# Kernel tuning notes

Hardware: AMD Instinct MI355X
Metric: run time of the kernel (lower is better)

## Reference

```python
import jax, jax.numpy as jnp
import numpy as np

B, T, C = 512, 256, 384  # batch, seq (<= block_size 256), n_embed
HEAD = 64


def setup_inputs() -> dict:
    key = jax.random.key(0)
    k1, k2, k3, k4 = jax.random.split(key, 4)
    scale = 1.0 / np.sqrt(C)
    return {
        "x": jax.random.normal(k1, (B, T, C), dtype=jnp.float32),
        "Wq": jax.random.normal(k2, (C, HEAD), dtype=jnp.float32) * scale,
        "Wk": jax.random.normal(k3, (C, HEAD), dtype=jnp.float32) * scale,
        "Wv": jax.random.normal(k4, (C, HEAD), dtype=jnp.float32) * scale,
    }


def reference(x, Wq, Wk, Wv):
    # Single causal self-attention head (dropout in eval mode / identity).
    _, T_, C_ = x.shape
    q = x @ Wq  # [B,T,H]
    k = x @ Wk  # [B,T,H]
    v = x @ Wv  # [B,T,H]
    # NOTE: original scales by n_embed**-0.5 (C), not head_size**-0.5.
    wei = jnp.einsum('bth,bsh->bts', q, k) * (C_ ** -0.5)  # [B,T,T]
    causal = jnp.tril(jnp.ones((T_, T_), dtype=bool))
    wei = jnp.where(causal, wei, -jnp.inf)
    wei = jax.nn.softmax(wei, axis=-1)
    return jnp.einsum('bts,bsh->bth', wei, v)  # [B,T,H]
```

## Files before the change

### kernel.cpp

```cpp
#include <hip/hip_runtime.h>

#define B_ 512
#define T_ 256
#define C_ 384
#define H_ 64

typedef __attribute__((ext_vector_type(8))) short bf16x8;
typedef __attribute__((ext_vector_type(4))) float f32x4;

__device__ __forceinline__ short f2bf(float f) {
    unsigned u = __float_as_uint(f);
    u += 0x7fffu + ((u >> 16) & 1u);
    return (short)(u >> 16);
}

__device__ __forceinline__ bf16x8 cvt8(const float* p) {
    const float4* p4 = (const float4*)p;
    float4 a = p4[0], b = p4[1];
    bf16x8 r;
    r[0] = f2bf(a.x); r[1] = f2bf(a.y); r[2] = f2bf(a.z); r[3] = f2bf(a.w);
    r[4] = f2bf(b.x); r[5] = f2bf(b.y); r[6] = f2bf(b.z); r[7] = f2bf(b.w);
    return r;
}

__global__ void pack_w_kernel(const float* __restrict__ Wq, const float* __restrict__ Wk,
                              const float* __restrict__ Wv, short* __restrict__ wp) {
    int p = blockIdx.x * 256 + threadIdx.x;
    if (p >= 12 * 12 * 512) return;
    int j    = p & 7;
    int lane = (p >> 3) & 63;
    int pc   = p >> 9;
    int ct = pc % 12, ks = pc / 12;
    int n  = ct * 16 + (lane & 15);
    int kk = ks * 32 + (lane >> 4) * 8 + j;
    const float* src = (n < 64) ? Wq : ((n < 128) ? Wk : Wv);
    wp[p] = f2bf(src[kk * 64 + (n & 63)]);
}

__global__ __launch_bounds__(256, 3) void qkv_kernel(
    const float* __restrict__ x, const short* __restrict__ wp,
    short* __restrict__ qo, short* __restrict__ ko, short* __restrict__ vo) {
    __shared__ short wtile[12 * 64 * 8];

    const int tid  = threadIdx.x;
    const int lane = tid & 63, w = tid >> 6;
    const int cl = lane & 15, quad = lane >> 4;
    const int rowbase = blockIdx.x * 128;

    const float* xr0 = x + (long)(rowbase + w * 32 + cl) * C_;
    const float* xr1 = xr0 + 16 * C_;

    f32x4 acc[2][12];
    #pragma unroll
    for (int rt = 0; rt < 2; rt++)
        #pragma unroll
        for (int ct = 0; ct < 12; ct++) {
            f32x4 z = {0.f, 0.f, 0.f, 0.f};
            acc[rt][ct] = z;
        }

    for (int ks = 0; ks < 12; ks++) {
        __syncthreads();
        const uint4* src = (const uint4*)(wp + ks * 6144);
        uint4* dst = (uint4*)wtile;
        #pragma unroll
        for (int i = 0; i < 3; i++)
            dst[tid + i * 256] = src[tid + i * 256];
        __syncthreads();

        const int koff = ks * 32 + quad * 8;
        bf16x8 a0 = cvt8(xr0 + koff);
        bf16x8 a1 = cvt8(xr1 + koff);
        #pragma unroll
        for (int ct = 0; ct < 12; ct++) {
            bf16x8 bf = *(const bf16x8*)(wtile + (ct * 64 + lane) * 8);
            acc[0][ct] = __builtin_amdgcn_mfma_f32_16x16x32_bf16(a0, bf, acc[0][ct], 0, 0, 0);
            acc[1][ct] = __builtin_amdgcn_mfma_f32_16x16x32_bf16(a1, bf, acc[1][ct], 0, 0, 0);
        }
    }

    #pragma unroll
    for (int rt = 0; rt < 2; rt++) {
        const int gb = rowbase + w * 32 + rt * 16 + quad * 4;
        #pragma unroll
        for (int ct = 0; ct < 12; ct++) {
            const int n = ct * 16 + cl;
            short* dstp = (n < 64) ? qo : ((n < 128) ? ko : vo);
            const int nn = n & 63;
            #pragma unroll
            for (int r = 0; r < 4; r++)
                dstp[(long)(gb + r) * 64 + nn] = f2bf(acc[rt][ct][r]);
        }
    }
}

__global__ __launch_bounds__(512, 4) void attn_kernel(
    const short* __restrict__ qi, const short* __restrict__ ki,
    const short* __restrict__ vi, float* __restrict__ out) {
    __shared__ short Vs[64 * 264];
    __shared__ short Pb[8][16 * 40];

    const int b = blockIdx.x;
    const int tid = threadIdx.x;
    const int w = tid >> 6, lane = tid & 63;
    const int cl = lane & 15, quad = lane >> 4;

    const short* vb = vi + b * (T_ * H_);
    for (int i = tid; i < (T_ * H_ / 4); i += 512) {
        const int e = i * 4;
        const int t = e >> 6, h = e & 63;
        short4 val = *(const short4*)(vb + e);
        Vs[(h + 0) * 264 + t] = val.x;
        Vs[(h + 1) * 264 + t] = val.y;
        Vs[(h + 2) * 264 + t] = val.z;
        Vs[(h + 3) * 264 + t] = val.w;
    }
    __syncthreads();

    const float scale = 0.05103103630798287f;

    for (int it = 0; it < 2; it++) {
        const int rg = it ? (15 - w) : w;
        const int base = rg << 4;

        const short* qb = qi + (long)(b * T_ + base + cl) * H_;
        const bf16x8 qf0 = *(const bf16x8*)(qb + quad * 8);
        const bf16x8 qf1 = *(const bf16x8*)(qb + 32 + quad * 8);

        f32x4 sacc[16];
        #pragma unroll
        for (int st = 0; st < 16; st++) {
            if (st > rg) continue;
            const short* kb = ki + (long)(b * T_ + st * 16 + cl) * H_;
            bf16x8 k0 = *(const bf16x8*)(kb + quad * 8);
            bf16x8 k1 = *(const bf16x8*)(kb + 32 + quad * 8);
            f32x4 z = {0.f, 0.f, 0.f, 0.f};
            f32x4 t = __builtin_amdgcn_mfma_f32_16x16x32_bf16(qf0, k0, z, 0, 0, 0);
            t = __builtin_amdgcn_mfma_f32_16x16x32_bf16(qf1, k1, t, 0, 0, 0);
            sacc[st] = t;
        }

        float m4[4] = {-3e38f, -3e38f, -3e38f, -3e38f};
        #pragma unroll
        for (int st = 0; st < 16; st++) {
            if (st > rg) continue;
            #pragma unroll
            for (int r = 0; r < 4; r++) {
                float sv = sacc[st][r] * scale;
                if (st * 16 + cl > base + quad * 4 + r) sv = -1e30f;
                sacc[st][r] = sv;
                m4[r] = fmaxf(m4[r], sv);
            }
        }
        #pragma unroll
        for (int d = 1; d < 16; d <<= 1)
            #pragma unroll
            for (int r = 0; r < 4; r++)
                m4[r] = fmaxf(m4[r], __shfl_xor(m4[r], d));

        float l4[4] = {0.f, 0.f, 0.f, 0.f};
        #pragma unroll
        for (int st = 0; st < 16; st++) {
            if (st > rg) continue;
            #pragma unroll
            for (int r = 0; r < 4; r++) {
                float pv = exp2f((sacc[st][r] - m4[r]) * 1.4426950408889634f);
                sacc[st][r] = pv;
                l4[r] += pv;
            }
        }
        #pragma unroll
        for (int d = 1; d < 16; d <<= 1)
            #pragma unroll
            for (int r = 0; r < 4; r++)
                l4[r] += __shfl_xor(l4[r], d);

        f32x4 oacc[4];
        #pragma unroll
        for (int ht = 0; ht < 4; ht++) {
            f32x4 z = {0.f, 0.f, 0.f, 0.f};
            oacc[ht] = z;
        }
        short* pb = Pb[w];
        #pragma unroll
        for (int c = 0; c < 8; c++) {
            if (c > (rg >> 1)) continue;
            #pragma unroll
            for (int half = 0; half < 2; half++) {
                const int st = c * 2 + half;
                #pragma unroll
                for (int r = 0; r < 4; r++) {
                    short pv = (st <= rg) ? f2bf(sacc[st][r]) : (short)0;
                    pb[(quad * 4 + r) * 40 + half * 16 + cl] = pv;
                }
            }
            __builtin_amdgcn_wave_barrier();
            const bf16x8 pa = *(const bf16x8*)(pb + cl * 40 + quad * 8);
            #pragma unroll
            for (int ht = 0; ht < 4; ht++) {
                const bf16x8 vf = *(const bf16x8*)(Vs + (ht * 16 + cl) * 264 + c * 32 + quad * 8);
                oacc[ht] = __builtin_amdgcn_mfma_f32_16x16x32_bf16(pa, vf, oacc[ht], 0, 0, 0);
            }
            __builtin_amdgcn_wave_barrier();
        }

        #pragma unroll
        for (int r = 0; r < 4; r++) {
            const float inv = 1.0f / l4[r];
            float* op = out + (long)(b * T_ + base + quad * 4 + r) * H_ + cl;
            #pragma unroll
            for (int ht = 0; ht < 4; ht++)
                op[ht * 16] = oacc[ht][r] * inv;
        }
    }
}

extern "C" void kernel_launch(void* const* d_in, const int* in_sizes, int n_in,
                              void* d_out, int out_size, void* d_ws, size_t ws_size,
                              hipStream_t stream) {
    const float* x  = (const float*)d_in[0];
    const float* Wq = (const float*)d_in[1];
    const float* Wk = (const float*)d_in[2];
    const float* Wv = (const float*)d_in[3];
    float* out = (float*)d_out;

    short* ws = (short*)d_ws;
    const long QKV = (long)B_ * T_ * H_;
    short* q  = ws;
    short* k  = ws + QKV;
    short* v  = ws + 2 * QKV;
    short* wp = ws + 3 * QKV;

    pack_w_kernel<<<288, 256, 0, stream>>>(Wq, Wk, Wv, wp);
    qkv_kernel<<<(B_ * T_) / 128, 256, 0, stream>>>(x, wp, q, k, v);
    attn_kernel<<<B_, 512, 0, stream>>>(q, k, v, out);
}
```

Before: 350.7 us.

## Split attention blocks per batch and read QKV weights directly from global

The QKV projection kernel drops its shared-memory weight staging and the two barriers per k-step, loading packed bf16 weight fragments straight from global/L2 instead. Its occupancy hint is lowered from 3 to 2 blocks. The attention kernel now runs two 256-thread blocks per batch, each handling half of the row groups, and the V transpose into LDS is rewritten to use vectorized shared-memory stores. This raises the block count and removes sync overhead, but it duplicates the V load and transpose across both blocks of a batch and may raise global load traffic in the projection.

```diff
diff --git a/kernel.cpp b/kernel.cpp
--- a/kernel.cpp
+++ b/kernel.cpp
@@ -37,11 +37,9 @@
     wp[p] = f2bf(src[kk * 64 + (n & 63)]);
 }
 
-__global__ __launch_bounds__(256, 3) void qkv_kernel(
+__global__ __launch_bounds__(256, 2) void qkv_kernel(
     const float* __restrict__ x, const short* __restrict__ wp,
     short* __restrict__ qo, short* __restrict__ ko, short* __restrict__ vo) {
-    __shared__ short wtile[12 * 64 * 8];
-
     const int tid  = threadIdx.x;
     const int lane = tid & 63, w = tid >> 6;
     const int cl = lane & 15, quad = lane >> 4;
@@ -59,21 +57,15 @@
             acc[rt][ct] = z;
         }
 
+    const short* wl = wp + lane * 8;
     for (int ks = 0; ks < 12; ks++) {
-        __syncthreads();
-        const uint4* src = (const uint4*)(wp + ks * 6144);
-        uint4* dst = (uint4*)wtile;
-        #pragma unroll
-        for (int i = 0; i < 3; i++)
-            dst[tid + i * 256] = src[tid + i * 256];
-        __syncthreads();
-
         const int koff = ks * 32 + quad * 8;
         bf16x8 a0 = cvt8(xr0 + koff);
         bf16x8 a1 = cvt8(xr1 + koff);
+        const short* wk = wl + ks * 6144;
         #pragma unroll
         for (int ct = 0; ct < 12; ct++) {
-            bf16x8 bf = *(const bf16x8*)(wtile + (ct * 64 + lane) * 8);
+            bf16x8 bf = *(const bf16x8*)(wk + ct * 512);
             acc[0][ct] = __builtin_amdgcn_mfma_f32_16x16x32_bf16(a0, bf, acc[0][ct], 0, 0, 0);
             acc[1][ct] = __builtin_amdgcn_mfma_f32_16x16x32_bf16(a1, bf, acc[1][ct], 0, 0, 0);
         }
@@ -94,33 +86,35 @@
     }
 }
 
-__global__ __launch_bounds__(512, 4) void attn_kernel(
+__global__ __launch_bounds__(256, 3) void attn_kernel(
     const short* __restrict__ qi, const short* __restrict__ ki,
     const short* __restrict__ vi, float* __restrict__ out) {
     __shared__ short Vs[64 * 264];
-    __shared__ short Pb[8][16 * 40];
-
-    const int b = blockIdx.x;
+    __shared__ short Pb[4][16 * 40];
+
+    const int b = blockIdx.x >> 1;
+    const int ph = blockIdx.x & 1;
     const int tid = threadIdx.x;
     const int w = tid >> 6, lane = tid & 63;
     const int cl = lane & 15, quad = lane >> 4;
 
     const short* vb = vi + b * (T_ * H_);
-    for (int i = tid; i < (T_ * H_ / 4); i += 512) {
-        const int e = i * 4;
-        const int t = e >> 6, h = e & 63;
-        short4 val = *(const short4*)(vb + e);
-        Vs[(h + 0) * 264 + t] = val.x;
-        Vs[(h + 1) * 264 + t] = val.y;
-        Vs[(h + 2) * 264 + t] = val.z;
-        Vs[(h + 3) * 264 + t] = val.w;
+    for (int i = tid; i < (T_ * H_ / 4); i += 256) {
+        const int h = i & 63, tg = i >> 6;
+        short4 val;
+        val.x = vb[(tg * 4 + 0) * 64 + h];
+        val.y = vb[(tg * 4 + 1) * 64 + h];
+        val.z = vb[(tg * 4 + 2) * 64 + h];
+        val.w = vb[(tg * 4 + 3) * 64 + h];
+        *(short4*)(Vs + h * 264 + tg * 4) = val;
     }
     __syncthreads();
 
     const float scale = 0.05103103630798287f;
 
     for (int it = 0; it < 2; it++) {
-        const int rg = it ? (15 - w) : w;
+        const int rg0 = ph * 4 + w;
+        const int rg = it ? (15 - rg0) : rg0;
         const int base = rg << 4;
 
         const short* qb = qi + (long)(b * T_ + base + cl) * H_;
@@ -233,5 +227,5 @@
 
     pack_w_kernel<<<288, 256, 0, stream>>>(Wq, Wk, Wv, wp);
     qkv_kernel<<<(B_ * T_) / 128, 256, 0, stream>>>(x, wp, q, k, v);
-    attn_kernel<<<B_, 512, 0, stream>>>(q, k, v, out);
-}
+    attn_kernel<<<B_ * 2, 256, 0, stream>>>(q, k, v, out);
+}
```

After: 357.7 us. About the same (+2.0%).
